# Performance work log

Measured on AMD Instinct MI355X. Metric: run time of the kernel, lower is better.

The kernel has to match this reference:

```python
import jax, jax.numpy as jnp
import numpy as np

B = 32768   # batch
D = 1024    # input_dimension
H = 2048    # hidden width (layer_sizes = [2048, 2048])
LN_EPS = 1e-5


def _layer_norm(h, g, b):
    m = jnp.mean(h, axis=-1, keepdims=True)
    v = jnp.var(h, axis=-1, keepdims=True)
    return (h - m) * jax.lax.rsqrt(v + LN_EPS) * g + b


def setup_inputs() -> dict:
    key = jax.random.key(0)
    ks = jax.random.split(key, 5)
    s1 = 1.0 / np.sqrt(D)
    s2 = 1.0 / np.sqrt(H)
    return {
        "x": jax.random.normal(ks[0], (B, D), dtype=jnp.float32),
        "W1": jax.random.uniform(ks[1], (D, H), jnp.float32, -s1, s1),
        "b1": jax.random.uniform(ks[2], (H,), jnp.float32, -s1, s1),
        "g1": jnp.ones((H,), jnp.float32),
        "be1": jnp.zeros((H,), jnp.float32),
        "W2": jax.random.uniform(ks[3], (H, 9), jnp.float32, -s2, s2),
        "b2": jax.random.uniform(ks[4], (9,), jnp.float32, -s2, s2),
        "g2": jnp.ones((9,), jnp.float32),
        "be2": jnp.zeros((9,), jnp.float32),
    }


def reference(x, W1, b1, g1, be1, W2, b2, g2, be2):
    # MLP: Linear -> ReLU -> LayerNorm, twice (final width 9)
    h = _layer_norm(jax.nn.relu(x @ W1 + b1), g1, be1)      # [B, H]
    r = _layer_norm(jax.nn.relu(h @ W2 + b2), g2, be2)      # [B, 9]
    R = r.reshape(x.shape[0], 3, 3)                          # [B, 3, 3]
    # SVD projection onto SO(3): U @ diag(1,1,det(U Vh)) @ Vh
    U, _, Vh = jnp.linalg.svd(R, full_matrices=False)
    d = jnp.linalg.det(U @ Vh)                               # [B]
    scale = jnp.stack([jnp.ones_like(d), jnp.ones_like(d), d], axis=-1)  # [B,3]
    return (U * scale[:, None, :]) @ Vh                      # scale last col of U
```

## Files before the change

kernel.cpp:

```cpp
#include <hip/hip_runtime.h>

typedef unsigned short u16;
typedef __bf16 bf16x8 __attribute__((ext_vector_type(8)));
typedef unsigned short us8 __attribute__((ext_vector_type(8)));
typedef float f32x4 __attribute__((ext_vector_type(4)));

#define GLD16(gptr, lptr)                                                              \
  __builtin_amdgcn_global_load_lds((const __attribute__((address_space(1))) void*)(gptr), \
                                   (__attribute__((address_space(3))) void*)(lptr), 16, 0, 0)

#define MFMA_BF16(a, b, c) __builtin_amdgcn_mfma_f32_16x16x32_bf16((a), (b), (c), 0, 0, 0)

static __device__ __forceinline__ u16 f2bf(float f) {
  unsigned int u = __float_as_uint(f);
  u += 0x7fffu + ((u >> 16) & 1u);
  return (u16)(u >> 16);
}
static __device__ __forceinline__ float bf2f(u16 h) {
  return __uint_as_float(((unsigned int)h) << 16);
}

__global__ __launch_bounds__(256) void k_split_x(const float* __restrict__ x,
                                                 u16* __restrict__ xh, u16* __restrict__ xl) {
  size_t i = (size_t)blockIdx.x * 256 + threadIdx.x;
  const float4* xf = (const float4*)x;
  float4 a = xf[2 * i], b = xf[2 * i + 1];
  float vv[8] = {a.x, a.y, a.z, a.w, b.x, b.y, b.z, b.w};
  us8 H, L;
#pragma unroll
  for (int j = 0; j < 8; ++j) {
    u16 hi = f2bf(vv[j]);
    H[j] = hi;
    L[j] = f2bf(vv[j] - bf2f(hi));
  }
  const int row = (int)(i >> 7);
  const int qp = ((int)i & 3) ^ ((row >> 1) & 3);
  const size_t dst = (i & ~(size_t)3) | (size_t)qp;
  *(us8*)(xh + dst * 8) = H;
  *(us8*)(xl + dst * 8) = L;
}

__global__ __launch_bounds__(256) void k_split_w1t(const float* __restrict__ w1,
                                                   u16* __restrict__ wh, u16* __restrict__ wl) {
  __shared__ float tile[32][33];
  int bn = blockIdx.x & 63;
  int bk = blockIdx.x >> 6;
  int tn = threadIdx.x & 31, tq = threadIdx.x >> 5;
#pragma unroll
  for (int r = 0; r < 4; ++r) {
    int k = bk * 32 + tq + r * 8;
    tile[tq + r * 8][tn] = w1[(size_t)k * 2048 + bn * 32 + tn];
  }
  __syncthreads();
#pragma unroll
  for (int r = 0; r < 4; ++r) {
    int n = bn * 32 + tq + r * 8;
    float v = tile[tn][tq + r * 8];
    u16 hi = f2bf(v);
    int qp = (tn >> 3) ^ ((n >> 1) & 3);
    int kp = bk * 32 + qp * 8 + (tn & 7);
    wh[(size_t)n * 1024 + kp] = hi;
    wl[(size_t)n * 1024 + kp] = f2bf(v - bf2f(hi));
  }
}

__global__ __launch_bounds__(256) void k_w2frag(const float* __restrict__ w2, const float* __restrict__ g1,
                                                u16* __restrict__ fh, u16* __restrict__ fl) {
  int t = blockIdx.x * 256 + threadIdx.x;
  int c = t >> 6, l = t & 63;
  int col = l & 15, lg = l >> 4;
  us8 H, L;
#pragma unroll
  for (int j = 0; j < 8; ++j) {
    int k = c * 32 + lg * 8 + j;
    float v = (col < 9) ? g1[k] * w2[k * 9 + col] : 0.f;
    u16 hi = f2bf(v);
    H[j] = hi;
    L[j] = f2bf(v - bf2f(hi));
  }
  *(us8*)(fh + (size_t)t * 8) = H;
  *(us8*)(fl + (size_t)t * 8) = L;
}

__global__ void k_cgcb(const float* __restrict__ w2, const float* __restrict__ g1,
                       const float* __restrict__ be1, double* __restrict__ cgcb) {
  int l = threadIdx.x;
  double cg[9], cb[9];
#pragma unroll
  for (int j = 0; j < 9; ++j) { cg[j] = 0.0; cb[j] = 0.0; }
  for (int i = 0; i < 32; ++i) {
    int k = i * 64 + l;
    double g = (double)g1[k], b = (double)be1[k];
#pragma unroll
    for (int j = 0; j < 9; ++j) {
      double w = (double)w2[k * 9 + j];
      cg[j] += g * w;
      cb[j] += b * w;
    }
  }
  for (int off = 32; off; off >>= 1) {
#pragma unroll
    for (int j = 0; j < 9; ++j) {
      cg[j] += __shfl_xor(cg[j], off, 64);
      cb[j] += __shfl_xor(cb[j], off, 64);
    }
  }
  if (l == 0) {
    for (int j = 0; j < 16; ++j) {
      cgcb[j] = (j < 9) ? cg[j] : 0.0;
      cgcb[16 + j] = (j < 9) ? cb[j] : 0.0;
    }
  }
}

__global__ __launch_bounds__(512, 2) void k_gemm1(const u16* __restrict__ xh, const u16* __restrict__ xl,
                                                  const u16* __restrict__ wh, const u16* __restrict__ wl,
                                                  const float* __restrict__ b1,
                                                  const u16* __restrict__ fh, const u16* __restrict__ fl,
                                                  float* __restrict__ pdot, float* __restrict__ pstat) {
  __shared__ __align__(16) u16 lds[2][4][8192];
  const int tid = threadIdx.x;
  const int swz = ((blockIdx.x & 7) << 7) | (blockIdx.x >> 3);
  const int m0 = (swz >> 3) << 8;
  const int n0 = (swz & 7) << 8;
  const int lane = tid & 63, w = tid >> 6;
  const int wr = (w >> 2) << 7;
  const int wc = (w & 3) << 6;
  const int lr = lane & 15, lg = lane >> 4;

  int a_off[8], b_off[4];
#pragma unroll
  for (int i = 0; i < 8; ++i) {
    int row = wr + i * 16 + lr;
    a_off[i] = row * 32 + ((lg ^ ((row >> 1) & 3)) << 3);
  }
#pragma unroll
  for (int j = 0; j < 4; ++j) {
    int row = wc + j * 16 + lr;
    b_off[j] = row * 32 + ((lg ^ ((row >> 1) & 3)) << 3);
  }

  const size_t aoff = (size_t)(m0 + (tid >> 2)) * 1024 + ((tid & 3) << 3);
  const size_t boff = (size_t)(n0 + (tid >> 2)) * 1024 + ((tid & 3) << 3);

#define STAGE1(bf, mt, src, off, kk)                          \
  do {                                                        \
    GLD16((src) + (off) + (kk), &lds[bf][mt][tid * 8]);       \
    GLD16((src) + (off) + 131072 + (kk), &lds[bf][mt][4096 + tid * 8]); \
  } while (0)

  STAGE1(0, 0, xh, aoff, 0);
  STAGE1(0, 1, xl, aoff, 0);
  STAGE1(0, 2, wh, boff, 0);
  STAGE1(0, 3, wl, boff, 0);

  f32x4 acc[8][4] = {};
#pragma unroll 2
  for (int kt = 0; kt < 32; ++kt) {
    const int cur = kt & 1, nxt = cur ^ 1;
    const int nk = (kt < 31 ? kt + 1 : 31) * 32;
    STAGE1(nxt, 0, xh, aoff, nk);
    asm volatile("s_waitcnt vmcnt(2)" ::: "memory");
    __builtin_amdgcn_s_barrier();
    asm volatile("" ::: "memory");
    const u16* Ah = &lds[cur][0][0];
    const u16* Al = &lds[cur][1][0];
    const u16* Bh = &lds[cur][2][0];
    const u16* Bl = &lds[cur][3][0];
    bf16x8 ahf[4], alf[4], bhf[4], blf[4];
#pragma unroll
    for (int j = 0; j < 4; ++j) {
      bhf[j] = *(const bf16x8*)(Bh + b_off[j]);
      blf[j] = *(const bf16x8*)(Bl + b_off[j]);
    }
#pragma unroll
    for (int i = 0; i < 4; ++i) {
      ahf[i] = *(const bf16x8*)(Ah + a_off[i]);
      alf[i] = *(const bf16x8*)(Al + a_off[i]);
    }
    STAGE1(nxt, 1, xl, aoff, nk);
    __builtin_amdgcn_s_setprio(1);
#pragma unroll
    for (int i = 0; i < 4; ++i)
#pragma unroll
      for (int j = 0; j < 2; ++j) {
        acc[i][j] = MFMA_BF16(ahf[i], bhf[j], acc[i][j]);
        acc[i][j] = MFMA_BF16(ahf[i], blf[j], acc[i][j]);
        acc[i][j] = MFMA_BF16(alf[i], bhf[j], acc[i][j]);
        acc[i][j] = MFMA_BF16(alf[i], blf[j], acc[i][j]);
      }
    __builtin_amdgcn_s_setprio(0);
    STAGE1(nxt, 2, wh, boff, nk);
    __builtin_amdgcn_s_setprio(1);
#pragma unroll
    for (int i = 0; i < 4; ++i)
#pragma unroll
      for (int j = 2; j < 4; ++j) {
        acc[i][j] = MFMA_BF16(ahf[i], bhf[j], acc[i][j]);
        acc[i][j] = MFMA_BF16(ahf[i], blf[j], acc[i][j]);
        acc[i][j] = MFMA_BF16(alf[i], bhf[j], acc[i][j]);
        acc[i][j] = MFMA_BF16(alf[i], blf[j], acc[i][j]);
      }
    __builtin_amdgcn_s_setprio(0);
    STAGE1(nxt, 3, wl, boff, nk);
#pragma unroll
    for (int i = 0; i < 4; ++i) {
      ahf[i] = *(const bf16x8*)(Ah + a_off[i + 4]);
      alf[i] = *(const bf16x8*)(Al + a_off[i + 4]);
    }
    __builtin_amdgcn_s_setprio(1);
#pragma unroll
    for (int i = 0; i < 4; ++i)
#pragma unroll
      for (int j = 0; j < 2; ++j) {
        acc[i + 4][j] = MFMA_BF16(ahf[i], bhf[j], acc[i + 4][j]);
        acc[i + 4][j] = MFMA_BF16(ahf[i], blf[j], acc[i + 4][j]);
        acc[i + 4][j] = MFMA_BF16(alf[i], bhf[j], acc[i + 4][j]);
        acc[i + 4][j] = MFMA_BF16(alf[i], blf[j], acc[i + 4][j]);
      }
    __builtin_amdgcn_s_setprio(0);
    __builtin_amdgcn_s_setprio(1);
#pragma unroll
    for (int i = 0; i < 4; ++i)
#pragma unroll
      for (int j = 2; j < 4; ++j) {
        acc[i + 4][j] = MFMA_BF16(ahf[i], bhf[j], acc[i + 4][j]);
        acc[i + 4][j] = MFMA_BF16(ahf[i], blf[j], acc[i + 4][j]);
        acc[i + 4][j] = MFMA_BF16(alf[i], bhf[j], acc[i + 4][j]);
        acc[i + 4][j] = MFMA_BF16(alf[i], blf[j], acc[i + 4][j]);
      }
    __builtin_amdgcn_s_setprio(0);
    asm volatile("" ::: "memory");
    __builtin_amdgcn_s_barrier();
  }
#undef STAGE1

  asm volatile("s_waitcnt vmcnt(0)" ::: "memory");
  __syncthreads();
  float* vt = (float*)&lds[0][0][0];

#pragma unroll
  for (int j = 0; j < 4; ++j) {
    const float bias = b1[n0 + wc + j * 16 + lr];
#pragma unroll
    for (int i = 0; i < 8; ++i)
#pragma unroll
      for (int r = 0; r < 4; ++r) acc[i][j][r] = fmaxf(acc[i][j][r] + bias, 0.f);
  }

  f32x4 acc2[2] = {};
  float sstat[2] = {0.f, 0.f}, qstat[2] = {0.f, 0.f};
  const int myrow0 = w * 32;

#pragma unroll
  for (int half = 0; half < 2; ++half) {
    if (((w & 3) >> 1) == half) {
      const int colbase = wc & 127;
#pragma unroll
      for (int j = 0; j < 4; ++j) {
        const int lcol = colbase + j * 16 + lr;
        const int g = lcol >> 2, wsel = lcol & 3;
#pragma unroll
        for (int i = 0; i < 8; ++i)
#pragma unroll
          for (int r = 0; r < 4; ++r) {
            const int row = wr + i * 16 + lg * 4 + r;
            vt[row * 128 + ((g ^ (row & 7)) << 2) + wsel] = acc[i][j][r];
          }
      }
    }
    __syncthreads();
#pragma unroll
    for (int cl = 0; cl < 4; ++cl) {
      const int cglob = (n0 >> 5) + half * 4 + cl;
      const bf16x8 bh = *(const bf16x8*)(fh + (size_t)(cglob * 64 + lane) * 8);
      const bf16x8 bl = *(const bf16x8*)(fl + (size_t)(cglob * 64 + lane) * 8);
#pragma unroll
      for (int g2 = 0; g2 < 2; ++g2) {
        const int row = myrow0 + g2 * 16 + lr;
        const int g0 = cl * 8 + lg * 2;
        const float4 f0 = *(const float4*)&vt[row * 128 + ((g0 ^ (row & 7)) << 2)];
        const float4 f1 = *(const float4*)&vt[row * 128 + (((g0 + 1) ^ (row & 7)) << 2)];
        float f[8] = {f0.x, f0.y, f0.z, f0.w, f1.x, f1.y, f1.z, f1.w};
        us8 HH, LL;
#pragma unroll
        for (int e = 0; e < 8; ++e) {
          sstat[g2] += f[e];
          qstat[g2] = fmaf(f[e], f[e], qstat[g2]);
          u16 hi = f2bf(f[e]);
          HH[e] = hi;
          LL[e] = f2bf(f[e] - bf2f(hi));
        }
        bf16x8 ah = __builtin_bit_cast(bf16x8, HH);
        bf16x8 al = __builtin_bit_cast(bf16x8, LL);
        acc2[g2] = MFMA_BF16(ah, bh, acc2[g2]);
        acc2[g2] = MFMA_BF16(ah, bl, acc2[g2]);
        acc2[g2] = MFMA_BF16(al, bh, acc2[g2]);
        acc2[g2] = MFMA_BF16(al, bl, acc2[g2]);
      }
    }
    __syncthreads();
  }

#pragma unroll
  for (int g2 = 0; g2 < 2; ++g2) {
    sstat[g2] += __shfl_xor(sstat[g2], 16, 64);
    sstat[g2] += __shfl_xor(sstat[g2], 32, 64);
    qstat[g2] += __shfl_xor(qstat[g2], 16, 64);
    qstat[g2] += __shfl_xor(qstat[g2], 32, 64);
  }
  const int ntile = n0 >> 8;
#pragma unroll
  for (int g2 = 0; g2 < 2; ++g2) {
    if (lg == 0) {
      const int row = m0 + myrow0 + g2 * 16 + lr;
      *(float2*)&pstat[((size_t)row * 8 + ntile) * 2] = make_float2(sstat[g2], qstat[g2]);
    }
    if (lr < 9) {
#pragma unroll
      for (int r = 0; r < 4; ++r) {
        const int row = m0 + myrow0 + g2 * 16 + lg * 4 + r;
        pdot[((size_t)row * 8 + ntile) * 12 + lr] = acc2[g2][r];
      }
    }
  }
}

static __device__ __forceinline__ void jrot(double S[3][3], double V[3][3], int p, int q, int r) {
  double apq = S[p][q];
  if (apq == 0.0) return;
  double tau = (S[q][q] - S[p][p]) / (2.0 * apq);
  double t = (tau >= 0.0 ? 1.0 : -1.0) / (fabs(tau) + sqrt(1.0 + tau * tau));
  double c = 1.0 / sqrt(1.0 + t * t);
  double s = t * c;
  double spp = S[p][p], sqq = S[q][q];
  double srp = S[r][p], srq = S[r][q];
  S[p][p] = spp - t * apq;
  S[q][q] = sqq + t * apq;
  S[p][q] = 0.0; S[q][p] = 0.0;
  S[r][p] = c * srp - s * srq; S[p][r] = S[r][p];
  S[r][q] = s * srp + c * srq; S[q][r] = S[r][q];
#pragma unroll
  for (int i = 0; i < 3; ++i) {
    double vip = V[i][p], viq = V[i][q];
    V[i][p] = c * vip - s * viq;
    V[i][q] = s * vip + c * viq;
  }
}

static __device__ void svd_so3(const double* Rf, float* Of) {
  double A[3][3], S[3][3];
  double V[3][3] = {{1, 0, 0}, {0, 1, 0}, {0, 0, 1}};
#pragma unroll
  for (int i = 0; i < 3; ++i)
#pragma unroll
    for (int j = 0; j < 3; ++j) A[i][j] = Rf[i * 3 + j];
#pragma unroll
  for (int p = 0; p < 3; ++p)
#pragma unroll
    for (int q = 0; q < 3; ++q) {
      double sa = 0.0;
#pragma unroll
      for (int i = 0; i < 3; ++i) sa += A[i][p] * A[i][q];
      S[p][q] = sa;
    }
  for (int it = 0; it < 6; ++it) {
    jrot(S, V, 0, 1, 2);
    jrot(S, V, 0, 2, 1);
    jrot(S, V, 1, 2, 0);
  }
  double l0 = S[0][0], l1 = S[1][1], l2 = S[2][2];
  double c0[3] = {V[0][0], V[1][0], V[2][0]};
  double c1[3] = {V[0][1], V[1][1], V[2][1]};
  double c2[3] = {V[0][2], V[1][2], V[2][2]};
  double tl, tv;
#define SWP(la, lb, ca, cb)                                         \
  if (la < lb) {                                                    \
    tl = la; la = lb; lb = tl;                                      \
    tv = ca[0]; ca[0] = cb[0]; cb[0] = tv;                          \
    tv = ca[1]; ca[1] = cb[1]; cb[1] = tv;                          \
    tv = ca[2]; ca[2] = cb[2]; cb[2] = tv;                          \
  }
  SWP(l0, l1, c0, c1)
  SWP(l0, l2, c0, c2)
  SWP(l1, l2, c1, c2)
#undef SWP
  double v3[3];
  v3[0] = c0[1] * c1[2] - c0[2] * c1[1];
  v3[1] = c0[2] * c1[0] - c0[0] * c1[2];
  v3[2] = c0[0] * c1[1] - c0[1] * c1[0];
  double t1[3], t2[3];
#pragma unroll
  for (int i = 0; i < 3; ++i) {
    t1[i] = A[i][0] * c0[0] + A[i][1] * c0[1] + A[i][2] * c0[2];
    t2[i] = A[i][0] * c1[0] + A[i][1] * c1[1] + A[i][2] * c1[2];
  }
  double n1 = sqrt(t1[0] * t1[0] + t1[1] * t1[1] + t1[2] * t1[2]);
  if (n1 < 1e-20) {
#pragma unroll
    for (int t = 0; t < 9; ++t) Of[t] = (t == 0 || t == 4 || t == 8) ? 1.f : 0.f;
    return;
  }
  double u1[3], u2[3], u3[3];
  double r1 = 1.0 / n1;
#pragma unroll
  for (int i = 0; i < 3; ++i) u1[i] = t1[i] * r1;
  double d12 = u1[0] * t2[0] + u1[1] * t2[1] + u1[2] * t2[2];
#pragma unroll
  for (int i = 0; i < 3; ++i) t2[i] -= d12 * u1[i];
  double n2 = sqrt(t2[0] * t2[0] + t2[1] * t2[1] + t2[2] * t2[2]);
  if (n2 > 1e-14 * n1) {
    double r2 = 1.0 / n2;
#pragma unroll
    for (int i = 0; i < 3; ++i) u2[i] = t2[i] * r2;
  } else {
    double ax = fabs(u1[0]), ay = fabs(u1[1]), az = fabs(u1[2]);
    double e[3] = {0.0, 0.0, 0.0};
    if (ax <= ay && ax <= az) e[0] = 1.0;
    else if (ay <= az) e[1] = 1.0;
    else e[2] = 1.0;
    double d = e[0] * u1[0] + e[1] * u1[1] + e[2] * u1[2];
#pragma unroll
    for (int i = 0; i < 3; ++i) e[i] -= d * u1[i];
    double nn = 1.0 / sqrt(e[0] * e[0] + e[1] * e[1] + e[2] * e[2]);
#pragma unroll
    for (int i = 0; i < 3; ++i) u2[i] = e[i] * nn;
  }
  u3[0] = u1[1] * u2[2] - u1[2] * u2[1];
  u3[1] = u1[2] * u2[0] - u1[0] * u2[2];
  u3[2] = u1[0] * u2[1] - u1[1] * u2[0];
#pragma unroll
  for (int i = 0; i < 3; ++i)
#pragma unroll
    for (int j = 0; j < 3; ++j)
      Of[i * 3 + j] = (float)(u1[i] * c0[j] + u2[i] * c1[j] + u3[i] * v3[j]);
}

__global__ __launch_bounds__(256) void k_comb(const float* __restrict__ pdot,
                                              const float* __restrict__ pstat,
                                              const double* __restrict__ cgcb,
                                              const float* __restrict__ b2,
                                              const float* __restrict__ g2v,
                                              const float* __restrict__ be2,
                                              float* __restrict__ out) {
  const int row = blockIdx.x * 256 + threadIdx.x;
  double dj[9];
#pragma unroll
  for (int j = 0; j < 9; ++j) dj[j] = 0.0;
  double s = 0.0, q = 0.0;
#pragma unroll
  for (int nt = 0; nt < 8; ++nt) {
    const float* p = pdot + ((size_t)row * 8 + nt) * 12;
#pragma unroll
    for (int j = 0; j < 9; ++j) dj[j] += (double)p[j];
    const float* ps = pstat + ((size_t)row * 8 + nt) * 2;
    s += (double)ps[0];
    q += (double)ps[1];
  }
  const double mean = s * (1.0 / 2048.0);
  const double varr = fmax(q * (1.0 / 2048.0) - mean * mean, 0.0);
  const double inv = 1.0 / sqrt(varr + 1e-5);
  double a2[9];
  double s9 = 0.0, q9 = 0.0;
#pragma unroll
  for (int j = 0; j < 9; ++j) {
    double v = inv * (dj[j] - mean * cgcb[j]) + cgcb[16 + j] + (double)b2[j];
    v = fmax(v, 0.0);
    a2[j] = v;
    s9 += v;
    q9 += v * v;
  }
  const double m2 = s9 * (1.0 / 9.0);
  const double v2c = fmax(q9 * (1.0 / 9.0) - m2 * m2, 0.0);
  const double i2 = 1.0 / sqrt(v2c + 1e-5);
  double rn[9];
#pragma unroll
  for (int j = 0; j < 9; ++j) rn[j] = (a2[j] - m2) * i2 * (double)g2v[j] + (double)be2[j];
  float O[9];
  svd_so3(rn, O);
  float* op = out + (size_t)row * 9;
#pragma unroll
  for (int t = 0; t < 9; ++t) op[t] = O[t];
}

extern "C" void kernel_launch(void* const* d_in, const int* in_sizes, int n_in,
                              void* d_out, int out_size, void* d_ws, size_t ws_size,
                              hipStream_t stream) {
  const float* x   = (const float*)d_in[0];
  const float* W1  = (const float*)d_in[1];
  const float* b1  = (const float*)d_in[2];
  const float* g1  = (const float*)d_in[3];
  const float* be1 = (const float*)d_in[4];
  const float* W2  = (const float*)d_in[5];
  const float* b2  = (const float*)d_in[6];
  const float* g2  = (const float*)d_in[7];
  const float* be2 = (const float*)d_in[8];
  float* out = (float*)d_out;
  char* ws = (char*)d_ws;
  u16*    xh   = (u16*)(ws + 0);
  u16*    xl   = (u16*)(ws + 67108864);
  u16*    wh   = (u16*)(ws + 134217728);
  u16*    wl   = (u16*)(ws + 138412032);
  u16*    fh   = (u16*)(ws + 142606336);
  u16*    fl   = (u16*)(ws + 142671872);
  double* cgcb = (double*)(ws + 142737408);
  float*  pdot = (float*)(ws + 142737664);
  float*  pstat= (float*)(ws + 155320576);

  k_split_x<<<dim3(16384), dim3(256), 0, stream>>>(x, xh, xl);
  k_split_w1t<<<dim3(2048), dim3(256), 0, stream>>>(W1, wh, wl);
  k_w2frag<<<dim3(16), dim3(256), 0, stream>>>(W2, g1, fh, fl);
  k_cgcb<<<dim3(1), dim3(64), 0, stream>>>(W2, g1, be1, cgcb);
  k_gemm1<<<dim3(1024), dim3(512), 0, stream>>>(xh, xl, wh, wl, b1, fh, fl, pdot, pstat);
  k_comb<<<dim3(128), dim3(256), 0, stream>>>(pdot, pstat, cgcb, b2, g2, be2, out);
}
```

Measured before the change: 457.6 us.

## Split GEMM k-step into four barrier-synced MFMA phases interleaved with LDS reads

Restructures the inner k-loop of the first GEMM into four phases. Each phase loads two A fragments from LDS, issues one of the next-tile global-to-LDS stages, waits on lgkmcnt, and runs 32 MFMAs between workgroup barriers. The aim is to keep waves in lockstep so LDS reads, global loads and MFMA bursts from different waves overlap in a ping-pong style, and to lower fragment register pressure. It adds several extra s_barriers per k-step, which could cost more than the overlap gains.

```diff
diff --git a/kernel.cpp b/kernel.cpp
--- a/kernel.cpp
+++ b/kernel.cpp
@@ -167,71 +167,44 @@
     const u16* Al = &lds[cur][1][0];
     const u16* Bh = &lds[cur][2][0];
     const u16* Bl = &lds[cur][3][0];
-    bf16x8 ahf[4], alf[4], bhf[4], blf[4];
-#pragma unroll
-    for (int j = 0; j < 4; ++j) {
-      bhf[j] = *(const bf16x8*)(Bh + b_off[j]);
-      blf[j] = *(const bf16x8*)(Bl + b_off[j]);
-    }
-#pragma unroll
-    for (int i = 0; i < 4; ++i) {
-      ahf[i] = *(const bf16x8*)(Ah + a_off[i]);
-      alf[i] = *(const bf16x8*)(Al + a_off[i]);
-    }
-    STAGE1(nxt, 1, xl, aoff, nk);
-    __builtin_amdgcn_s_setprio(1);
-#pragma unroll
-    for (int i = 0; i < 4; ++i)
-#pragma unroll
-      for (int j = 0; j < 2; ++j) {
-        acc[i][j] = MFMA_BF16(ahf[i], bhf[j], acc[i][j]);
-        acc[i][j] = MFMA_BF16(ahf[i], blf[j], acc[i][j]);
-        acc[i][j] = MFMA_BF16(alf[i], bhf[j], acc[i][j]);
-        acc[i][j] = MFMA_BF16(alf[i], blf[j], acc[i][j]);
-      }
-    __builtin_amdgcn_s_setprio(0);
-    STAGE1(nxt, 2, wh, boff, nk);
-    __builtin_amdgcn_s_setprio(1);
-#pragma unroll
-    for (int i = 0; i < 4; ++i)
-#pragma unroll
-      for (int j = 2; j < 4; ++j) {
-        acc[i][j] = MFMA_BF16(ahf[i], bhf[j], acc[i][j]);
-        acc[i][j] = MFMA_BF16(ahf[i], blf[j], acc[i][j]);
-        acc[i][j] = MFMA_BF16(alf[i], bhf[j], acc[i][j]);
-        acc[i][j] = MFMA_BF16(alf[i], blf[j], acc[i][j]);
-      }
-    __builtin_amdgcn_s_setprio(0);
-    STAGE1(nxt, 3, wl, boff, nk);
-#pragma unroll
-    for (int i = 0; i < 4; ++i) {
-      ahf[i] = *(const bf16x8*)(Ah + a_off[i + 4]);
-      alf[i] = *(const bf16x8*)(Al + a_off[i + 4]);
-    }
-    __builtin_amdgcn_s_setprio(1);
-#pragma unroll
-    for (int i = 0; i < 4; ++i)
-#pragma unroll
-      for (int j = 0; j < 2; ++j) {
-        acc[i + 4][j] = MFMA_BF16(ahf[i], bhf[j], acc[i + 4][j]);
-        acc[i + 4][j] = MFMA_BF16(ahf[i], blf[j], acc[i + 4][j]);
-        acc[i + 4][j] = MFMA_BF16(alf[i], bhf[j], acc[i + 4][j]);
-        acc[i + 4][j] = MFMA_BF16(alf[i], blf[j], acc[i + 4][j]);
-      }
-    __builtin_amdgcn_s_setprio(0);
-    __builtin_amdgcn_s_setprio(1);
-#pragma unroll
-    for (int i = 0; i < 4; ++i)
-#pragma unroll
-      for (int j = 2; j < 4; ++j) {
-        acc[i + 4][j] = MFMA_BF16(ahf[i], bhf[j], acc[i + 4][j]);
-        acc[i + 4][j] = MFMA_BF16(ahf[i], blf[j], acc[i + 4][j]);
-        acc[i + 4][j] = MFMA_BF16(alf[i], bhf[j], acc[i + 4][j]);
-        acc[i + 4][j] = MFMA_BF16(alf[i], blf[j], acc[i + 4][j]);
-      }
-    __builtin_amdgcn_s_setprio(0);
-    asm volatile("" ::: "memory");
-    __builtin_amdgcn_s_barrier();
+    bf16x8 bhf[4], blf[4];
+#pragma unroll
+    for (int p = 0; p < 4; ++p) {
+      if (p == 0) {
+#pragma unroll
+        for (int j = 0; j < 4; ++j) {
+          bhf[j] = *(const bf16x8*)(Bh + b_off[j]);
+          blf[j] = *(const bf16x8*)(Bl + b_off[j]);
+        }
+      }
+      bf16x8 ah0 = *(const bf16x8*)(Ah + a_off[2 * p]);
+      bf16x8 al0 = *(const bf16x8*)(Al + a_off[2 * p]);
+      bf16x8 ah1 = *(const bf16x8*)(Ah + a_off[2 * p + 1]);
+      bf16x8 al1 = *(const bf16x8*)(Al + a_off[2 * p + 1]);
+      if (p == 0) STAGE1(nxt, 1, xl, aoff, nk);
+      if (p == 1) STAGE1(nxt, 2, wh, boff, nk);
+      if (p == 2) STAGE1(nxt, 3, wl, boff, nk);
+      __builtin_amdgcn_s_barrier();
+      asm volatile("s_waitcnt lgkmcnt(0)" ::: "memory");
+      __builtin_amdgcn_sched_barrier(0);
+      __builtin_amdgcn_s_setprio(1);
+#pragma unroll
+      for (int j = 0; j < 4; ++j) {
+        acc[2 * p][j] = MFMA_BF16(ah0, bhf[j], acc[2 * p][j]);
+        acc[2 * p][j] = MFMA_BF16(ah0, blf[j], acc[2 * p][j]);
+        acc[2 * p][j] = MFMA_BF16(al0, bhf[j], acc[2 * p][j]);
+        acc[2 * p][j] = MFMA_BF16(al0, blf[j], acc[2 * p][j]);
+      }
+#pragma unroll
+      for (int j = 0; j < 4; ++j) {
+        acc[2 * p + 1][j] = MFMA_BF16(ah1, bhf[j], acc[2 * p + 1][j]);
+        acc[2 * p + 1][j] = MFMA_BF16(ah1, blf[j], acc[2 * p + 1][j]);
+        acc[2 * p + 1][j] = MFMA_BF16(al1, bhf[j], acc[2 * p + 1][j]);
+        acc[2 * p + 1][j] = MFMA_BF16(al1, blf[j], acc[2 * p + 1][j]);
+      }
+      __builtin_amdgcn_s_setprio(0);
+      __builtin_amdgcn_s_barrier();
+    }
   }
 #undef STAGE1
 
```

Result: slower. 470.0 us (+2.7%).

## Shrink GEMM1 block tile from 256x256 to 128x128 with 4 waves

Applied to the files above, without the earlier changes.

The first GEMM now uses 128x128 output tiles per block with 256 threads (4 waves of 64x64) instead of 256x256 tiles with 512 threads. That gives 4096 blocks, half the LDS per block and half the accumulator registers, so more blocks can be resident. The fused second-layer epilogue now handles a single 128-column chunk, so there are 16 partial tiles per row and the combine kernel sums over 16 instead of 8. The trade-off is less operand reuse per block, which roughly doubles the global and L2 traffic for A and B, plus larger partial buffers.

```diff
diff --git a/kernel.cpp b/kernel.cpp
--- a/kernel.cpp
+++ b/kernel.cpp
@@ -113,24 +113,24 @@
   }
 }
 
-__global__ __launch_bounds__(512, 2) void k_gemm1(const u16* __restrict__ xh, const u16* __restrict__ xl,
+__global__ __launch_bounds__(256, 2) void k_gemm1(const u16* __restrict__ xh, const u16* __restrict__ xl,
                                                   const u16* __restrict__ wh, const u16* __restrict__ wl,
                                                   const float* __restrict__ b1,
                                                   const u16* __restrict__ fh, const u16* __restrict__ fl,
                                                   float* __restrict__ pdot, float* __restrict__ pstat) {
-  __shared__ __align__(16) u16 lds[2][4][8192];
+  __shared__ __align__(16) u16 lds[2][4][4096];
   const int tid = threadIdx.x;
-  const int swz = ((blockIdx.x & 7) << 7) | (blockIdx.x >> 3);
-  const int m0 = (swz >> 3) << 8;
-  const int n0 = (swz & 7) << 8;
+  const int swz = ((blockIdx.x & 7) << 9) | (blockIdx.x >> 3);
+  const int m0 = (swz >> 4) << 7;
+  const int n0 = (swz & 15) << 7;
   const int lane = tid & 63, w = tid >> 6;
-  const int wr = (w >> 2) << 7;
-  const int wc = (w & 3) << 6;
+  const int wr = (w >> 1) << 6;
+  const int wc = (w & 1) << 6;
   const int lr = lane & 15, lg = lane >> 4;
 
-  int a_off[8], b_off[4];
-#pragma unroll
-  for (int i = 0; i < 8; ++i) {
+  int a_off[4], b_off[4];
+#pragma unroll
+  for (int i = 0; i < 4; ++i) {
     int row = wr + i * 16 + lr;
     a_off[i] = row * 32 + ((lg ^ ((row >> 1) & 3)) << 3);
   }
@@ -146,7 +146,7 @@
 #define STAGE1(bf, mt, src, off, kk)                          \
   do {                                                        \
     GLD16((src) + (off) + (kk), &lds[bf][mt][tid * 8]);       \
-    GLD16((src) + (off) + 131072 + (kk), &lds[bf][mt][4096 + tid * 8]); \
+    GLD16((src) + (off) + 65536 + (kk), &lds[bf][mt][2048 + tid * 8]); \
   } while (0)
 
   STAGE1(0, 0, xh, aoff, 0);
@@ -154,7 +154,7 @@
   STAGE1(0, 2, wh, boff, 0);
   STAGE1(0, 3, wl, boff, 0);
 
-  f32x4 acc[8][4] = {};
+  f32x4 acc[4][4] = {};
 #pragma unroll 2
   for (int kt = 0; kt < 32; ++kt) {
     const int cur = kt & 1, nxt = cur ^ 1;
@@ -181,9 +181,9 @@
     STAGE1(nxt, 1, xl, aoff, nk);
     __builtin_amdgcn_s_setprio(1);
 #pragma unroll
-    for (int i = 0; i < 4; ++i)
-#pragma unroll
-      for (int j = 0; j < 2; ++j) {
+    for (int i = 0; i < 2; ++i)
+#pragma unroll
+      for (int j = 0; j < 4; ++j) {
         acc[i][j] = MFMA_BF16(ahf[i], bhf[j], acc[i][j]);
         acc[i][j] = MFMA_BF16(ahf[i], blf[j], acc[i][j]);
         acc[i][j] = MFMA_BF16(alf[i], bhf[j], acc[i][j]);
@@ -193,42 +193,22 @@
     STAGE1(nxt, 2, wh, boff, nk);
     __builtin_amdgcn_s_setprio(1);
 #pragma unroll
-    for (int i = 0; i < 4; ++i)
-#pragma unroll
-      for (int j = 2; j < 4; ++j) {
-        acc[i][j] = MFMA_BF16(ahf[i], bhf[j], acc[i][j]);
-        acc[i][j] = MFMA_BF16(ahf[i], blf[j], acc[i][j]);
-        acc[i][j] = MFMA_BF16(alf[i], bhf[j], acc[i][j]);
-        acc[i][j] = MFMA_BF16(alf[i], blf[j], acc[i][j]);
-      }
+    for (int j = 0; j < 4; ++j) {
+      acc[2][j] = MFMA_BF16(ahf[2], bhf[j], acc[2][j]);
+      acc[2][j] = MFMA_BF16(ahf[2], blf[j], acc[2][j]);
+      acc[2][j] = MFMA_BF16(alf[2], bhf[j], acc[2][j]);
+      acc[2][j] = MFMA_BF16(alf[2], blf[j], acc[2][j]);
+    }
     __builtin_amdgcn_s_setprio(0);
     STAGE1(nxt, 3, wl, boff, nk);
-#pragma unroll
-    for (int i = 0; i < 4; ++i) {
-      ahf[i] = *(const bf16x8*)(Ah + a_off[i + 4]);
-      alf[i] = *(const bf16x8*)(Al + a_off[i + 4]);
-    }
     __builtin_amdgcn_s_setprio(1);
 #pragma unroll
-    for (int i = 0; i < 4; ++i)
-#pragma unroll
-      for (int j = 0; j < 2; ++j) {
-        acc[i + 4][j] = MFMA_BF16(ahf[i], bhf[j], acc[i + 4][j]);
-        acc[i + 4][j] = MFMA_BF16(ahf[i], blf[j], acc[i + 4][j]);
-        acc[i + 4][j] = MFMA_BF16(alf[i], bhf[j], acc[i + 4][j]);
-        acc[i + 4][j] = MFMA_BF16(alf[i], blf[j], acc[i + 4][j]);
-      }
-    __builtin_amdgcn_s_setprio(0);
-    __builtin_amdgcn_s_setprio(1);
-#pragma unroll
-    for (int i = 0; i < 4; ++i)
-#pragma unroll
-      for (int j = 2; j < 4; ++j) {
-        acc[i + 4][j] = MFMA_BF16(ahf[i], bhf[j], acc[i + 4][j]);
-        acc[i + 4][j] = MFMA_BF16(ahf[i], blf[j], acc[i + 4][j]);
-        acc[i + 4][j] = MFMA_BF16(alf[i], bhf[j], acc[i + 4][j]);
-        acc[i + 4][j] = MFMA_BF16(alf[i], blf[j], acc[i + 4][j]);
-      }
+    for (int j = 0; j < 4; ++j) {
+      acc[3][j] = MFMA_BF16(ahf[3], bhf[j], acc[3][j]);
+      acc[3][j] = MFMA_BF16(ahf[3], blf[j], acc[3][j]);
+      acc[3][j] = MFMA_BF16(alf[3], bhf[j], acc[3][j]);
+      acc[3][j] = MFMA_BF16(alf[3], blf[j], acc[3][j]);
+    }
     __builtin_amdgcn_s_setprio(0);
     asm volatile("" ::: "memory");
     __builtin_amdgcn_s_barrier();
@@ -243,63 +223,56 @@
   for (int j = 0; j < 4; ++j) {
     const float bias = b1[n0 + wc + j * 16 + lr];
 #pragma unroll
-    for (int i = 0; i < 8; ++i)
+    for (int i = 0; i < 4; ++i)
 #pragma unroll
       for (int r = 0; r < 4; ++r) acc[i][j][r] = fmaxf(acc[i][j][r] + bias, 0.f);
   }
+
+#pragma unroll
+  for (int j = 0; j < 4; ++j) {
+    const int lcol = wc + j * 16 + lr;
+    const int g = lcol >> 2, wsel = lcol & 3;
+#pragma unroll
+    for (int i = 0; i < 4; ++i)
+#pragma unroll
+      for (int r = 0; r < 4; ++r) {
+        const int row = wr + i * 16 + lg * 4 + r;
+        vt[row * 128 + ((g ^ (row & 7)) << 2) + wsel] = acc[i][j][r];
+      }
+  }
+  __syncthreads();
 
   f32x4 acc2[2] = {};
   float sstat[2] = {0.f, 0.f}, qstat[2] = {0.f, 0.f};
   const int myrow0 = w * 32;
-
-#pragma unroll
-  for (int half = 0; half < 2; ++half) {
-    if (((w & 3) >> 1) == half) {
-      const int colbase = wc & 127;
-#pragma unroll
-      for (int j = 0; j < 4; ++j) {
-        const int lcol = colbase + j * 16 + lr;
-        const int g = lcol >> 2, wsel = lcol & 3;
-#pragma unroll
-        for (int i = 0; i < 8; ++i)
-#pragma unroll
-          for (int r = 0; r < 4; ++r) {
-            const int row = wr + i * 16 + lg * 4 + r;
-            vt[row * 128 + ((g ^ (row & 7)) << 2) + wsel] = acc[i][j][r];
-          }
+#pragma unroll
+  for (int cl = 0; cl < 4; ++cl) {
+    const int cglob = (n0 >> 5) + cl;
+    const bf16x8 bh = *(const bf16x8*)(fh + (size_t)(cglob * 64 + lane) * 8);
+    const bf16x8 bl = *(const bf16x8*)(fl + (size_t)(cglob * 64 + lane) * 8);
+#pragma unroll
+    for (int g2 = 0; g2 < 2; ++g2) {
+      const int row = myrow0 + g2 * 16 + lr;
+      const int g0 = cl * 8 + lg * 2;
+      const float4 f0 = *(const float4*)&vt[row * 128 + ((g0 ^ (row & 7)) << 2)];
+      const float4 f1 = *(const float4*)&vt[row * 128 + (((g0 + 1) ^ (row & 7)) << 2)];
+      float f[8] = {f0.x, f0.y, f0.z, f0.w, f1.x, f1.y, f1.z, f1.w};
+      us8 HH, LL;
+#pragma unroll
+      for (int e = 0; e < 8; ++e) {
+        sstat[g2] += f[e];
+        qstat[g2] = fmaf(f[e], f[e], qstat[g2]);
+        u16 hi = f2bf(f[e]);
+        HH[e] = hi;
+        LL[e] = f2bf(f[e] - bf2f(hi));
       }
-    }
-    __syncthreads();
-#pragma unroll
-    for (int cl = 0; cl < 4; ++cl) {
-      const int cglob = (n0 >> 5) + half * 4 + cl;
-      const bf16x8 bh = *(const bf16x8*)(fh + (size_t)(cglob * 64 + lane) * 8);
-      const bf16x8 bl = *(const bf16x8*)(fl + (size_t)(cglob * 64 + lane) * 8);
-#pragma unroll
-      for (int g2 = 0; g2 < 2; ++g2) {
-        const int row = myrow0 + g2 * 16 + lr;
-        const int g0 = cl * 8 + lg * 2;
-        const float4 f0 = *(const float4*)&vt[row * 128 + ((g0 ^ (row & 7)) << 2)];
-        const float4 f1 = *(const float4*)&vt[row * 128 + (((g0 + 1) ^ (row & 7)) << 2)];
-        float f[8] = {f0.x, f0.y, f0.z, f0.w, f1.x, f1.y, f1.z, f1.w};
-        us8 HH, LL;
-#pragma unroll
-        for (int e = 0; e < 8; ++e) {
-          sstat[g2] += f[e];
-          qstat[g2] = fmaf(f[e], f[e], qstat[g2]);
-          u16 hi = f2bf(f[e]);
-          HH[e] = hi;
-          LL[e] = f2bf(f[e] - bf2f(hi));
-        }
-        bf16x8 ah = __builtin_bit_cast(bf16x8, HH);
-        bf16x8 al = __builtin_bit_cast(bf16x8, LL);
-        acc2[g2] = MFMA_BF16(ah, bh, acc2[g2]);
-        acc2[g2] = MFMA_BF16(ah, bl, acc2[g2]);
-        acc2[g2] = MFMA_BF16(al, bh, acc2[g2]);
-        acc2[g2] = MFMA_BF16(al, bl, acc2[g2]);
-      }
-    }
-    __syncthreads();
+      bf16x8 ah = __builtin_bit_cast(bf16x8, HH);
+      bf16x8 al = __builtin_bit_cast(bf16x8, LL);
+      acc2[g2] = MFMA_BF16(ah, bh, acc2[g2]);
+      acc2[g2] = MFMA_BF16(ah, bl, acc2[g2]);
+      acc2[g2] = MFMA_BF16(al, bh, acc2[g2]);
+      acc2[g2] = MFMA_BF16(al, bl, acc2[g2]);
+    }
   }
 
 #pragma unroll
@@ -309,18 +282,18 @@
     qstat[g2] += __shfl_xor(qstat[g2], 16, 64);
     qstat[g2] += __shfl_xor(qstat[g2], 32, 64);
   }
-  const int ntile = n0 >> 8;
+  const int ntile = n0 >> 7;
 #pragma unroll
   for (int g2 = 0; g2 < 2; ++g2) {
     if (lg == 0) {
       const int row = m0 + myrow0 + g2 * 16 + lr;
-      *(float2*)&pstat[((size_t)row * 8 + ntile) * 2] = make_float2(sstat[g2], qstat[g2]);
+      *(float2*)&pstat[((size_t)row * 16 + ntile) * 2] = make_float2(sstat[g2], qstat[g2]);
     }
     if (lr < 9) {
 #pragma unroll
       for (int r = 0; r < 4; ++r) {
         const int row = m0 + myrow0 + g2 * 16 + lg * 4 + r;
-        pdot[((size_t)row * 8 + ntile) * 12 + lr] = acc2[g2][r];
+        pdot[((size_t)row * 16 + ntile) * 12 + lr] = acc2[g2][r];
       }
     }
   }
@@ -449,11 +422,11 @@
   for (int j = 0; j < 9; ++j) dj[j] = 0.0;
   double s = 0.0, q = 0.0;
 #pragma unroll
-  for (int nt = 0; nt < 8; ++nt) {
-    const float* p = pdot + ((size_t)row * 8 + nt) * 12;
+  for (int nt = 0; nt < 16; ++nt) {
+    const float* p = pdot + ((size_t)row * 16 + nt) * 12;
 #pragma unroll
     for (int j = 0; j < 9; ++j) dj[j] += (double)p[j];
-    const float* ps = pstat + ((size_t)row * 8 + nt) * 2;
+    const float* ps = pstat + ((size_t)row * 16 + nt) * 2;
     s += (double)ps[0];
     q += (double)ps[1];
   }
@@ -505,12 +478,12 @@
   u16*    fl   = (u16*)(ws + 142671872);
   double* cgcb = (double*)(ws + 142737408);
   float*  pdot = (float*)(ws + 142737664);
-  float*  pstat= (float*)(ws + 155320576);
+  float*  pstat= (float*)(ws + 167903488);
 
   k_split_x<<<dim3(16384), dim3(256), 0, stream>>>(x, xh, xl);
   k_split_w1t<<<dim3(2048), dim3(256), 0, stream>>>(W1, wh, wl);
   k_w2frag<<<dim3(16), dim3(256), 0, stream>>>(W2, g1, fh, fl);
   k_cgcb<<<dim3(1), dim3(64), 0, stream>>>(W2, g1, be1, cgcb);
-  k_gemm1<<<dim3(1024), dim3(512), 0, stream>>>(xh, xl, wh, wl, b1, fh, fl, pdot, pstat);
+  k_gemm1<<<dim3(4096), dim3(256), 0, stream>>>(xh, xl, wh, wl, b1, fh, fl, pdot, pstat);
   k_comb<<<dim3(128), dim3(256), 0, stream>>>(pdot, pstat, cgcb, b2, g2, be2, out);
 }
```

New measurement: 509.8 us. 11.4% more time.
